# Kernel tuning notes

Measured on AMD Instinct MI355X. Metric: run time of the kernel, lower is better.

Reference implementation:

```python
import jax, jax.numpy as jnp
import numpy as np

B, S, D = 4, 2048, 1024


def setup_inputs() -> dict:
    key = jax.random.key(0)
    ks = jax.random.split(key, 10)
    scale = 1.0 / np.sqrt(D)
    x = jax.random.normal(ks[0], (B, S, D), dtype=jnp.float32)
    # causal mask [B, S, S]: 1 where attendable, 0 where masked
    mask = jnp.broadcast_to(jnp.tril(jnp.ones((S, S), dtype=jnp.int32)), (B, S, S))
    Wq = jax.random.normal(ks[1], (D, D), dtype=jnp.float32) * scale
    bq = jnp.zeros((D,), dtype=jnp.float32)
    Wk = jax.random.normal(ks[2], (D, D), dtype=jnp.float32) * scale
    bk = jnp.zeros((D,), dtype=jnp.float32)
    Wv = jax.random.normal(ks[3], (D, D), dtype=jnp.float32) * scale
    bv = jnp.zeros((D,), dtype=jnp.float32)
    Wo = jax.random.normal(ks[4], (D, D), dtype=jnp.float32) * scale
    bo = jnp.zeros((D,), dtype=jnp.float32)
    return {"x": x, "mask": mask, "Wq": Wq, "bq": bq, "Wk": Wk, "bk": bk,
            "Wv": Wv, "bv": bv, "Wo": Wo, "bo": bo}


def reference(x, mask, Wq, bq, Wk, bk, Wv, bv, Wo, bo):
    d_k = x.shape[-1]
    inv_std = 1.0 / jnp.sqrt(jnp.asarray(d_k, x.dtype))
    q = x @ Wq + bq                                   # [B,S,D]
    k = x @ Wk + bk                                   # [B,S,D]
    v = x @ Wv + bv                                   # [B,S,D]
    scores = jnp.einsum('bqd,bkd->bqk', q, k) * inv_std  # [B,S,S]
    # masked_fill(mask[:, -q_len:, :] == 0, -inf); q_len == S here
    scores = jnp.where(mask == 0, jnp.asarray(-jnp.inf, scores.dtype), scores)
    attn = jax.nn.softmax(scores, axis=-1)
    # dropout p=0 (eval) -> identity
    ctx = jnp.einsum('bqk,bkd->bqd', attn, v)         # [B,S,D]
    out = ctx @ Wo + bo
    return out
```

## Files before the change

kernel.cpp:

```cpp
#include <hip/hip_runtime.h>
#include <hip/hip_bf16.h>


typedef __bf16 bf16x8 __attribute__((ext_vector_type(8)));
typedef __bf16 bf16x4 __attribute__((ext_vector_type(4)));
typedef float  f32x4  __attribute__((ext_vector_type(4)));

#define BDIM 1024
#define SDIM 2048
#define BATCH 4

#define BAR()  do { asm volatile("" ::: "memory"); __builtin_amdgcn_s_barrier(); \
                    asm volatile("" ::: "memory"); } while (0)

__device__ __forceinline__ void gload_lds16(const void* g, void* l) {
    __builtin_amdgcn_global_load_lds(
        (const __attribute__((address_space(1))) void*)g,
        (__attribute__((address_space(3))) void*)l, 16, 0, 0);
}

__global__ __launch_bounds__(256) void prepass(const float* __restrict__ x,
                                               const float* __restrict__ Wq,
                                               const float* __restrict__ Wk,
                                               const float* __restrict__ Wv,
                                               const float* __restrict__ Wo,
                                               const float* __restrict__ bq,
                                               const float* __restrict__ bk,
                                               const float* __restrict__ bv,
                                               __bf16* __restrict__ xb,
                                               __bf16* __restrict__ Wcat,
                                               __bf16* __restrict__ Wot,
                                               float* __restrict__ bcat) {
    const int bid = blockIdx.x;
    const int tid = threadIdx.x;
    if (bid < 8192) {
        const long i = ((long)bid * 256 + tid) * 4;
        const float4 v = *(const float4*)(x + i);
        bf16x4 o;
        o[0] = (__bf16)v.x; o[1] = (__bf16)v.y; o[2] = (__bf16)v.z; o[3] = (__bf16)v.w;
        *(bf16x4*)(xb + i) = o;
    } else if (bid < 12288) {
        __shared__ float tile[32][33];
        const int b2 = bid - 8192;
        const int w = b2 >> 10, t = b2 & 1023;
        const int r0 = (t >> 5) * 32, c0 = (t & 31) * 32;
        const float* src = (w == 0) ? Wq : (w == 1) ? Wk : (w == 2) ? Wv : Wo;
        __bf16* dst = (w < 3) ? (Wcat + (long)w * 1048576) : Wot;
        const int tx = tid & 31, ty = tid >> 5;
        #pragma unroll
        for (int j = ty; j < 32; j += 8)
            tile[j][tx] = src[(long)(r0 + j) * 1024 + (c0 + tx)];
        __syncthreads();
        #pragma unroll
        for (int j = ty; j < 32; j += 8)
            dst[(long)(c0 + j) * 1024 + (r0 + tx)] = (__bf16)tile[tx][j];
    } else {
        const int i = (bid - 12288) * 256 + tid;
        if (i < 3072)
            bcat[i] = (i < 1024) ? bq[i] : ((i < 2048) ? bk[i - 1024] : bv[i - 2048]);
    }
}

template <typename Tout, int BN, bool CSKIP, bool PVMODE, bool SWZ, bool VTOUT>
__global__ __launch_bounds__(512, 1) void gemm2p(const __bf16* __restrict__ Ag,
                                                 const __bf16* __restrict__ Bg,
                                                 Tout* __restrict__ C0,
                                                 __bf16* __restrict__ M16,
                                                 __bf16* __restrict__ E1,
                                                 __bf16* __restrict__ Cd,
                                                 __bf16* __restrict__ Vt,
                                                 const float* __restrict__ bias,
                                                 int K, int lda, int ldb, int ldc,
                                                 int nbx, long sA, long sB, long sC) {
    constexpr int NF = BN / 64;
    constexpr int NB = BN / 64;
    int bx, by;
    const int bz = blockIdx.z;
    if (SWZ) {
        const int flat = blockIdx.x;
        const int w = (flat & 7) * ((int)gridDim.x >> 3) + (flat >> 3);
        bx = w % nbx; by = w / nbx;
    } else { bx = blockIdx.x; by = blockIdx.y; }
    if (CSKIP && bx * BN > by * 256 + 255) return;

    const int m0 = by * 256, n0 = bx * BN;
    int kStart = 0, kEnd = K;
    const __bf16* A; const __bf16* B;
    Tout* C = nullptr;
    __bf16* Wout = nullptr;
    int rShift = 0;
    if (PVMODE) {
        const int b = bz >> 1, ch = bz & 1;
        kStart = ch << 10;
        kEnd = min((by + 1) * 256, kStart + 1024);
        if (kEnd <= kStart) return;
        A = Ag + (long)b * sA;
        B = Bg + (long)b * sB;
        if (ch == 0) {
            if (by < 4) { rShift = 0;    Wout = Cd  + (long)b * sC; }
            else        { rShift = 1024; Wout = M16 + (long)b * 1048576; }
        } else          { rShift = 1024; Wout = E1  + (long)b * 1048576; }
    } else {
        A = Ag + (long)bz * sA;
        B = Bg + (long)bz * sB;
        C = C0 + (long)bz * sC;
    }
    const int NT = (kEnd - kStart) >> 6;

    __shared__ __align__(16) char smem[65536 + BN * 256];

    const int tid = threadIdx.x;
    const int wid = tid >> 6, l = tid & 63;
    const int wm = wid >> 2, wn = wid & 3;
    const int lr = l & 15, lu = l >> 4;

    int srcA[4], srcB[NB];
    #pragma unroll
    for (int i = 0; i < 4; ++i) {
        const int beta = i * 8192 + tid * 16;
        const int r = beta >> 7;
        const int cb = (beta & 127) ^ ((r & 7) << 4);
        srcA[i] = (m0 + r) * lda + (cb >> 1);
    }
    #pragma unroll
    for (int i = 0; i < NB; ++i) {
        const int beta = i * 8192 + tid * 16;
        const int r = beta >> 7;
        const int cb = (beta & 127) ^ ((r & 7) << 4);
        srcB[i] = (n0 + r) * ldb + (cb >> 1);
    }
    auto stage = [&](int buf, int koff) {
        #pragma unroll
        for (int i = 0; i < 4; ++i)
            gload_lds16(A + srcA[i] + koff,
                        smem + buf * 32768 + i * 8192 + wid * 1024);
        #pragma unroll
        for (int j = 0; j < NB; ++j)
            gload_lds16(B + srcB[j] + koff,
                        smem + 65536 + buf * (BN * 128) + j * 8192 + wid * 1024);
    };

    const int xo  = (lr & 7) << 4;
    const int c0e = ((lu << 4) ^ xo) >> 1;
    const int c1e = ((64 + (lu << 4)) ^ xo) >> 1;
    const int aLo = (wm * 64 + lr) * 64;
    const int aHi = (128 + wm * 64 + lr) * 64;
    const int bBase = (wn * (BN / 4) + lr) * 64;

    f32x4 acc[8][NF] = {};

    stage(0, kStart);
    asm volatile("s_waitcnt vmcnt(0)" ::: "memory");
    BAR();

    for (int T = 0; T < NT; ++T) {
        const int c = T & 1;
        const bool more = (T + 1 < NT);
        if (more) stage(c ^ 1, kStart + (T + 1) * 64);

        const __bf16* Ab = (const __bf16*)(smem + c * 32768);
        const __bf16* Bb = (const __bf16*)(smem + 65536 + c * (BN * 128));
        #pragma unroll
        for (int kk = 0; kk < 2; ++kk) {
            const int ce = kk ? c1e : c0e;
            bf16x8 aR[8], bR[NF];
            #pragma unroll
            for (int m = 0; m < 4; ++m) {
                aR[m]     = *(const bf16x8*)(Ab + aLo + m * 1024 + ce);
                aR[4 + m] = *(const bf16x8*)(Ab + aHi + m * 1024 + ce);
            }
            #pragma unroll
            for (int n = 0; n < NF; ++n)
                bR[n] = *(const bf16x8*)(Bb + bBase + n * 1024 + ce);
            #pragma unroll
            for (int m = 0; m < 8; ++m)
                #pragma unroll
                for (int n = 0; n < NF; ++n)
                    acc[m][n] = __builtin_amdgcn_mfma_f32_16x16x32_bf16(
                        aR[m], bR[n], acc[m][n], 0, 0, 0);
        }

        if (more) {
            asm volatile("s_waitcnt vmcnt(0)" ::: "memory");
            BAR();
        }
    }

    const int rb = lu * 4, cl = lr;

    #pragma unroll
    for (int n = 0; n < NF; ++n) {
        const int col = n0 + wn * (BN / 4) + n * 16 + cl;
        if (VTOUT && col >= 2048) continue;
        const float bvv = bias ? bias[col] : 0.f;
        #pragma unroll
        for (int mi = 0; mi < 8; ++mi) {
            const int row = m0 + (mi >> 2) * 128 + wm * 64 + (mi & 3) * 16 + rb;
            #pragma unroll
            for (int r = 0; r < 4; ++r) {
                const float v = acc[mi][n][r] + bvv;
                if constexpr (PVMODE)
                    Wout[(long)(row + r - rShift) * ldc + col] = (__bf16)v;
                else
                    C[(long)(row + r) * ldc + col] = (Tout)v;
            }
        }
    }

    if constexpr (VTOUT) {
        const bool hasV = (n0 + BN > 2048);
        if (hasV) {
            __syncthreads();
            #pragma unroll
            for (int n = 0; n < NF; ++n) {
                const int col = n0 + wn * (BN / 4) + n * 16 + cl;
                if (col < 2048) continue;
                const int lcol = wn * (BN / 4) + n * 16 + cl;
                const float bvv = bias ? bias[col] : 0.f;
                #pragma unroll
                for (int mi = 0; mi < 8; ++mi) {
                    const int rl = (mi >> 2) * 128 + wm * 64 + (mi & 3) * 16 + rb;
                    bf16x4 o;
                    #pragma unroll
                    for (int r = 0; r < 4; ++r) o[r] = (__bf16)(acc[mi][n][r] + bvv);
                    *(bf16x4*)(smem + lcol * 528 + rl * 2) = o;
                }
            }
            __syncthreads();
            const int vStart = (n0 >= 2048) ? 0 : (2048 - n0);
            const int nV = BN - vStart;
            const int bb = m0 >> 11, s0 = m0 & 2047;
            for (int t = tid; t < nV * 32; t += 512) {
                const int ddl = vStart + (t >> 5);
                const int sl = (t & 31) * 8;
                const bf16x8 v = *(const bf16x8*)(smem + ddl * 528 + sl * 2);
                *(bf16x8*)(Vt + (long)bb * 2097152 +
                           (long)(n0 + ddl - 2048) * 2048 + s0 + sl) = v;
            }
        }
    }
}

__global__ __launch_bounds__(256) void merge2(const __bf16* __restrict__ M16,
                                              const __bf16* __restrict__ E1,
                                              __bf16* __restrict__ out) {
    const long i = ((long)blockIdx.x * 256 + threadIdx.x) * 8;
    const long b = i >> 20;
    const long j = i & 1048575;
    const bf16x8 a = *(const bf16x8*)(M16 + b * 1048576 + j);
    const bf16x8 c = *(const bf16x8*)(E1 + b * 1048576 + j);
    bf16x8 o;
    #pragma unroll
    for (int t = 0; t < 8; ++t) o[t] = (__bf16)((float)a[t] + (float)c[t]);
    *(bf16x8*)(out + b * 2097152 + 1048576 + j) = o;
}

__global__ __launch_bounds__(256) void softmax_causal(const __bf16* __restrict__ scores,
                                                      __bf16* __restrict__ P, float scale) {
    const int q = blockIdx.x;
    const long b = blockIdx.y;
    const __bf16* srow = scores + (b * SDIM + q) * (long)SDIM;
    __bf16* prow = P + (b * SDIM + q) * (long)SDIM;
    const int n = q + 1;
    const int kBound = ((q >> 8) + 1) << 8;
    const int tid = threadIdx.x;
    const int k0 = tid * 8;
    __shared__ float red[8];

    float vals[8];
    float mx = -1e30f;
    if (k0 < n) {
        const bf16x8 v = *(const bf16x8*)(srow + k0);
        #pragma unroll
        for (int i = 0; i < 8; ++i) {
            const float s = (k0 + i < n) ? (float)v[i] * scale : -1e30f;
            vals[i] = s;
            mx = fmaxf(mx, s);
        }
    } else {
        #pragma unroll
        for (int i = 0; i < 8; ++i) vals[i] = -1e30f;
    }
    #pragma unroll
    for (int o = 32; o > 0; o >>= 1) mx = fmaxf(mx, __shfl_xor(mx, o));
    if ((tid & 63) == 0) red[tid >> 6] = mx;
    __syncthreads();
    mx = fmaxf(fmaxf(red[0], red[1]), fmaxf(red[2], red[3]));

    float p[8];
    float sum = 0.f;
    #pragma unroll
    for (int i = 0; i < 8; ++i) {
        p[i] = __expf(vals[i] - mx);
        sum += p[i];
    }
    #pragma unroll
    for (int o = 32; o > 0; o >>= 1) sum += __shfl_xor(sum, o);
    if ((tid & 63) == 0) red[4 + (tid >> 6)] = sum;
    __syncthreads();
    sum = red[4] + red[5] + red[6] + red[7];

    if (k0 < kBound) {
        const float inv = 1.f / sum;
        bf16x8 o;
        #pragma unroll
        for (int i = 0; i < 8; ++i)
            o[i] = (__bf16)((k0 + i < n) ? p[i] * inv : 0.f);
        *(bf16x8*)(prow + k0) = o;
    }
}

extern "C" void kernel_launch(void* const* d_in, const int* in_sizes, int n_in,
                              void* d_out, int out_size, void* d_ws, size_t ws_size,
                              hipStream_t stream) {
    const float* x  = (const float*)d_in[0];
    const float* Wq = (const float*)d_in[2];
    const float* bq = (const float*)d_in[3];
    const float* Wk = (const float*)d_in[4];
    const float* bk = (const float*)d_in[5];
    const float* Wv = (const float*)d_in[6];
    const float* bv = (const float*)d_in[7];
    const float* Wo = (const float*)d_in[8];
    const float* bo = (const float*)d_in[9];
    float* out = (float*)d_out;

    char* ws = (char*)d_ws;
    const long XE = (long)BATCH * SDIM * BDIM;
    __bf16* xb    = (__bf16*)(ws);
    __bf16* Wcat  = (__bf16*)(ws + 16777216);
    __bf16* Wot   = (__bf16*)(ws + 23068672);
    float*  bcat  = (float*)(ws + 25165824);
    __bf16* QKVb  = (__bf16*)(ws + 25178112);
    __bf16* Vtb   = (__bf16*)(ws + 75509760);
    __bf16* Sc    = (__bf16*)(ws + 92286976);
    __bf16* Pb    = (__bf16*)(ws + 25178112);
    __bf16* M16   = (__bf16*)(ws + 92286976);
    __bf16* E1    = (__bf16*)(ws + 100675584);
    __bf16* ctxb  = (__bf16*)(ws + 58732544);

    const long SD  = (long)SDIM * BDIM;
    const long SS  = (long)SDIM * SDIM;
    const long SQ3 = (long)SDIM * 3 * BDIM;

    prepass<<<dim3(12300), 256, 0, stream>>>(x, Wq, Wk, Wv, Wo, bq, bk, bv,
                                             xb, Wcat, Wot, bcat);

    gemm2p<__bf16, 192, false, false, true, true><<<dim3(512, 1, 1), 512, 0, stream>>>(
        xb, Wcat, QKVb, nullptr, nullptr, nullptr, Vtb, bcat,
        BDIM, BDIM, BDIM, 3072, 16, 0, 0, 0);
    gemm2p<__bf16, 256, true, false, false, false><<<dim3(8, 8, BATCH), 512, 0, stream>>>(
        QKVb, QKVb + 1024, Sc, nullptr, nullptr, nullptr, nullptr, nullptr,
        BDIM, 3072, 3072, SDIM, 8, SQ3, SQ3, SS);
    softmax_causal<<<dim3(SDIM, BATCH), 256, 0, stream>>>(Sc, Pb, 0.03125f);
    gemm2p<__bf16, 256, false, true, false, false><<<dim3(4, 8, 2 * BATCH), 512, 0, stream>>>(
        Pb, Vtb, nullptr, M16, E1, ctxb, nullptr, nullptr,
        SDIM, SDIM, SDIM, BDIM, 4, SS, SD, SD);
    merge2<<<dim3((unsigned)(BATCH * 1048576 / 8 / 256)), 256, 0, stream>>>(
        M16, E1, ctxb);
    gemm2p<float, 128, false, false, true, false><<<dim3(256, 1, 1), 512, 0, stream>>>(
        ctxb, Wot, out, nullptr, nullptr, nullptr, nullptr, bo,
        BDIM, BDIM, BDIM, BDIM, 8, 0, 0, 0);
}
```

Measured before the change: 182.5 us.

## Fuse exponentiation into the score GEMM and defer softmax normalization to PV

Removes the separate softmax kernel. The QK^T GEMM epilogue now writes exp(score*scale) with the causal mask applied. A light rowsum kernel computes the inverse row sums, and the PV GEMM epilogue scales its partial outputs by them. This cuts one full read and write pass over the score matrix, but it drops the max-subtraction, so exp can overflow if scores are large. Workspace buffers are also reassigned.

```diff
diff --git a/kernel.cpp b/kernel.cpp
--- a/kernel.cpp
+++ b/kernel.cpp
@@ -61,7 +61,8 @@
     }
 }
 
-template <typename Tout, int BN, bool CSKIP, bool PVMODE, bool SWZ, bool VTOUT>
+template <typename Tout, int BN, bool CSKIP, bool PVMODE, bool SWZ, bool VTOUT,
+          bool EXPOUT>
 __global__ __launch_bounds__(512, 1) void gemm2p(const __bf16* __restrict__ Ag,
                                                  const __bf16* __restrict__ Bg,
                                                  Tout* __restrict__ C0,
@@ -70,6 +71,7 @@
                                                  __bf16* __restrict__ Cd,
                                                  __bf16* __restrict__ Vt,
                                                  const float* __restrict__ bias,
+                                                 const float* __restrict__ invSum,
                                                  int K, int lda, int ldb, int ldc,
                                                  int nbx, long sA, long sB, long sC) {
     constexpr int NF = BN / 64;
@@ -88,6 +90,7 @@
     const __bf16* A; const __bf16* B;
     Tout* C = nullptr;
     __bf16* Wout = nullptr;
+    const float* invS = nullptr;
     int rShift = 0;
     if (PVMODE) {
         const int b = bz >> 1, ch = bz & 1;
@@ -96,6 +99,7 @@
         if (kEnd <= kStart) return;
         A = Ag + (long)b * sA;
         B = Bg + (long)b * sB;
+        invS = invSum + (long)b * SDIM;
         if (ch == 0) {
             if (by < 4) { rShift = 0;    Wout = Cd  + (long)b * sC; }
             else        { rShift = 1024; Wout = M16 + (long)b * 1048576; }
@@ -198,11 +202,16 @@
             const int row = m0 + (mi >> 2) * 128 + wm * 64 + (mi & 3) * 16 + rb;
             #pragma unroll
             for (int r = 0; r < 4; ++r) {
-                const float v = acc[mi][n][r] + bvv;
-                if constexpr (PVMODE)
+                float v = acc[mi][n][r] + bvv;
+                if constexpr (EXPOUT) {
+                    const float e = (col <= row + r) ? __expf(v * 0.03125f) : 0.f;
+                    C[(long)(row + r) * ldc + col] = (Tout)e;
+                } else if constexpr (PVMODE) {
+                    v *= invS[row + r];
                     Wout[(long)(row + r - rShift) * ldc + col] = (__bf16)v;
-                else
+                } else {
                     C[(long)(row + r) * ldc + col] = (Tout)v;
+                }
             }
         }
     }
@@ -241,6 +250,30 @@
     }
 }
 
+__global__ __launch_bounds__(256) void rowsum_inv(const __bf16* __restrict__ P,
+                                                  float* __restrict__ invSum) {
+    const int q = blockIdx.x;
+    const long b = blockIdx.y;
+    const __bf16* prow = P + (b * SDIM + q) * (long)SDIM;
+    const int kBound = ((q >> 8) + 1) << 8;
+    const int tid = threadIdx.x;
+    const int k0 = tid * 8;
+    __shared__ float red[4];
+
+    float sum = 0.f;
+    if (k0 < kBound) {
+        const bf16x8 v = *(const bf16x8*)(prow + k0);
+        #pragma unroll
+        for (int i = 0; i < 8; ++i) sum += (float)v[i];
+    }
+    #pragma unroll
+    for (int o = 32; o > 0; o >>= 1) sum += __shfl_xor(sum, o);
+    if ((tid & 63) == 0) red[tid >> 6] = sum;
+    __syncthreads();
+    if (tid == 0)
+        invSum[b * SDIM + q] = 1.f / (red[0] + red[1] + red[2] + red[3]);
+}
+
 __global__ __launch_bounds__(256) void merge2(const __bf16* __restrict__ M16,
                                               const __bf16* __restrict__ E1,
                                               __bf16* __restrict__ out) {
@@ -253,61 +286,6 @@
     #pragma unroll
     for (int t = 0; t < 8; ++t) o[t] = (__bf16)((float)a[t] + (float)c[t]);
     *(bf16x8*)(out + b * 2097152 + 1048576 + j) = o;
-}
-
-__global__ __launch_bounds__(256) void softmax_causal(const __bf16* __restrict__ scores,
-                                                      __bf16* __restrict__ P, float scale) {
-    const int q = blockIdx.x;
-    const long b = blockIdx.y;
-    const __bf16* srow = scores + (b * SDIM + q) * (long)SDIM;
-    __bf16* prow = P + (b * SDIM + q) * (long)SDIM;
-    const int n = q + 1;
-    const int kBound = ((q >> 8) + 1) << 8;
-    const int tid = threadIdx.x;
-    const int k0 = tid * 8;
-    __shared__ float red[8];
-
-    float vals[8];
-    float mx = -1e30f;
-    if (k0 < n) {
-        const bf16x8 v = *(const bf16x8*)(srow + k0);
-        #pragma unroll
-        for (int i = 0; i < 8; ++i) {
-            const float s = (k0 + i < n) ? (float)v[i] * scale : -1e30f;
-            vals[i] = s;
-            mx = fmaxf(mx, s);
-        }
-    } else {
-        #pragma unroll
-        for (int i = 0; i < 8; ++i) vals[i] = -1e30f;
-    }
-    #pragma unroll
-    for (int o = 32; o > 0; o >>= 1) mx = fmaxf(mx, __shfl_xor(mx, o));
-    if ((tid & 63) == 0) red[tid >> 6] = mx;
-    __syncthreads();
-    mx = fmaxf(fmaxf(red[0], red[1]), fmaxf(red[2], red[3]));
-
-    float p[8];
-    float sum = 0.f;
-    #pragma unroll
-    for (int i = 0; i < 8; ++i) {
-        p[i] = __expf(vals[i] - mx);
-        sum += p[i];
-    }
-    #pragma unroll
-    for (int o = 32; o > 0; o >>= 1) sum += __shfl_xor(sum, o);
-    if ((tid & 63) == 0) red[4 + (tid >> 6)] = sum;
-    __syncthreads();
-    sum = red[4] + red[5] + red[6] + red[7];
-
-    if (k0 < kBound) {
-        const float inv = 1.f / sum;
-        bf16x8 o;
-        #pragma unroll
-        for (int i = 0; i < 8; ++i)
-            o[i] = (__bf16)((k0 + i < n) ? p[i] * inv : 0.f);
-        *(bf16x8*)(prow + k0) = o;
-    }
 }
 
 extern "C" void kernel_launch(void* const* d_in, const int* in_sizes, int n_in,
@@ -325,17 +303,16 @@
     float* out = (float*)d_out;
 
     char* ws = (char*)d_ws;
-    const long XE = (long)BATCH * SDIM * BDIM;
     __bf16* xb    = (__bf16*)(ws);
     __bf16* Wcat  = (__bf16*)(ws + 16777216);
     __bf16* Wot   = (__bf16*)(ws + 23068672);
     float*  bcat  = (float*)(ws + 25165824);
     __bf16* QKVb  = (__bf16*)(ws + 25178112);
     __bf16* Vtb   = (__bf16*)(ws + 75509760);
-    __bf16* Sc    = (__bf16*)(ws + 92286976);
-    __bf16* Pb    = (__bf16*)(ws + 25178112);
-    __bf16* M16   = (__bf16*)(ws + 92286976);
-    __bf16* E1    = (__bf16*)(ws + 100675584);
+    __bf16* Pb    = (__bf16*)(ws + 92286976);
+    __bf16* M16   = (__bf16*)(ws);
+    __bf16* E1    = (__bf16*)(ws + 8388608);
+    float*  invSum= (float*)(ws + 16777216);
     __bf16* ctxb  = (__bf16*)(ws + 58732544);
 
     const long SD  = (long)SDIM * BDIM;
@@ -345,19 +322,23 @@
     prepass<<<dim3(12300), 256, 0, stream>>>(x, Wq, Wk, Wv, Wo, bq, bk, bv,
                                              xb, Wcat, Wot, bcat);
 
-    gemm2p<__bf16, 192, false, false, true, true><<<dim3(512, 1, 1), 512, 0, stream>>>(
-        xb, Wcat, QKVb, nullptr, nullptr, nullptr, Vtb, bcat,
+    gemm2p<__bf16, 192, false, false, true, true, false>
+        <<<dim3(512, 1, 1), 512, 0, stream>>>(
+        xb, Wcat, QKVb, nullptr, nullptr, nullptr, Vtb, bcat, nullptr,
         BDIM, BDIM, BDIM, 3072, 16, 0, 0, 0);
-    gemm2p<__bf16, 256, true, false, false, false><<<dim3(8, 8, BATCH), 512, 0, stream>>>(
-        QKVb, QKVb + 1024, Sc, nullptr, nullptr, nullptr, nullptr, nullptr,
+    gemm2p<__bf16, 256, true, false, false, false, true>
+        <<<dim3(8, 8, BATCH), 512, 0, stream>>>(
+        QKVb, QKVb + 1024, Pb, nullptr, nullptr, nullptr, nullptr, nullptr, nullptr,
         BDIM, 3072, 3072, SDIM, 8, SQ3, SQ3, SS);
-    softmax_causal<<<dim3(SDIM, BATCH), 256, 0, stream>>>(Sc, Pb, 0.03125f);
-    gemm2p<__bf16, 256, false, true, false, false><<<dim3(4, 8, 2 * BATCH), 512, 0, stream>>>(
-        Pb, Vtb, nullptr, M16, E1, ctxb, nullptr, nullptr,
+    rowsum_inv<<<dim3(SDIM, BATCH), 256, 0, stream>>>(Pb, invSum);
+    gemm2p<__bf16, 256, false, true, false, false, false>
+        <<<dim3(4, 8, 2 * BATCH), 512, 0, stream>>>(
+        Pb, Vtb, nullptr, M16, E1, ctxb, nullptr, nullptr, invSum,
         SDIM, SDIM, SDIM, BDIM, 4, SS, SD, SD);
     merge2<<<dim3((unsigned)(BATCH * 1048576 / 8 / 256)), 256, 0, stream>>>(
         M16, E1, ctxb);
-    gemm2p<float, 128, false, false, true, false><<<dim3(256, 1, 1), 512, 0, stream>>>(
-        ctxb, Wot, out, nullptr, nullptr, nullptr, nullptr, bo,
+    gemm2p<float, 128, false, false, true, false, false>
+        <<<dim3(256, 1, 1), 512, 0, stream>>>(
+        ctxb, Wot, out, nullptr, nullptr, nullptr, nullptr, bo, nullptr,
         BDIM, BDIM, BDIM, BDIM, 8, 0, 0, 0);
 }
```

Result: no change. 182.7 us (+0.1%).
